# Kernel optimization log

Hardware: AMD Instinct MI355X
Metric: run time of the kernel (lower is better)

Reference implementation:

```python
import jax, jax.numpy as jnp
import numpy as np

B, N, C = 2, 4096, 512
NUM_HEADS = 8
HEAD_DIM = C // NUM_HEADS
SCALE = HEAD_DIM ** -0.5
THETA = 10000.0


def setup_inputs() -> dict:
    key = jax.random.key(0)
    ks = jax.random.split(key, 5)
    x = jax.random.normal(ks[0], (B, N, C), dtype=jnp.float32)
    Wqkv = jax.random.normal(ks[1], (3 * C, C), dtype=jnp.float32) * 0.02
    bqkv = jax.random.normal(ks[2], (3 * C,), dtype=jnp.float32) * 0.02
    Wproj = jax.random.normal(ks[3], (C, C), dtype=jnp.float32) * 0.02
    bproj = jax.random.normal(ks[4], (C,), dtype=jnp.float32) * 0.02
    return {"x": x, "Wqkv": Wqkv, "bqkv": bqkv, "Wproj": Wproj, "bproj": bproj}


def _rope(x, seq_len, head_dim):
    # x: [B, H, N, head_dim]; interleaved rotary embedding
    freqs = 1.0 / THETA ** (jnp.arange(0, head_dim, 2, dtype=jnp.float32) / head_dim)  # [hd/2]
    t = jnp.arange(seq_len, dtype=jnp.float32)
    freqs_cis = jnp.outer(t, freqs)                      # [N, hd/2]
    sin_f = jnp.sin(freqs_cis)
    cos_f = jnp.cos(freqs_cis)
    x_even = x[..., ::2]                                 # [B, H, N, hd/2]
    x_odd = x[..., 1::2]
    rot = jnp.stack(
        [x_even * cos_f - x_odd * sin_f,
         x_even * sin_f + x_odd * cos_f],
        axis=-1,
    )                                                    # [B, H, N, hd/2, 2]
    return rot.reshape(x.shape)


def reference(x, Wqkv, bqkv, Wproj, bproj):
    b, n, c = x.shape
    # fused QKV projection: y = x @ W.T + b
    qkv = x @ Wqkv.T + bqkv                              # [B, N, 3C]
    qkv = qkv.reshape(b, n, 3, NUM_HEADS, HEAD_DIM)
    qkv = jnp.transpose(qkv, (2, 0, 3, 1, 4))            # [3, B, H, N, hd]
    q, k, v = qkv[0], qkv[1], qkv[2]
    q = _rope(q, n, HEAD_DIM)
    k = _rope(k, n, HEAD_DIM)
    attn = jnp.einsum('bhqd,bhkd->bhqk', q, k) * SCALE   # [B, H, N, N]
    attn = jax.nn.softmax(attn, axis=-1)
    out = jnp.einsum('bhqk,bhkd->bhqd', attn, v)         # [B, H, N, hd]
    out = jnp.transpose(out, (0, 2, 1, 3)).reshape(b, n, c)
    return out @ Wproj.T + bproj
```

## Files before the change

### kernel.cpp

```cpp
#include <hip/hip_runtime.h>
#include <hip/hip_bf16.h>
#include <stdint.h>

#define B_ 2
#define N_ 4096
#define C_ 512
#define H_ 8
#define D_ 64
#define M_ (B_*N_)
#define K3_ (3*C_)
#define NCH 2

typedef __attribute__((ext_vector_type(8)))  short short8;
typedef __attribute__((ext_vector_type(4)))  float f32x4;
typedef __attribute__((ext_vector_type(16))) float f32x16;

static __device__ __forceinline__ unsigned short f2bf(float f) {
  union { float f; unsigned u; } cv; cv.f = f;
  unsigned r = cv.u + 0x7fffu + ((cv.u >> 16) & 1u);
  return (unsigned short)(r >> 16);
}
static __device__ __forceinline__ float bf2f(short x) {
  union { unsigned u; float f; } cv;
  cv.u = ((unsigned)(unsigned short)x) << 16;
  return cv.f;
}
static __device__ __forceinline__ float fexp2(float x) {
#if __has_builtin(__builtin_amdgcn_exp2f)
  return __builtin_amdgcn_exp2f(x);
#else
  return exp2f(x);
#endif
}
static __device__ __forceinline__ unsigned cvt_pk_bf16(float a, float b) {
  unsigned r;
  asm("v_cvt_pk_bf16_f32 %0, %1, %2" : "=v"(r) : "v"(a), "v"(b));
  return r;
}
static __device__ __forceinline__ void gload_lds16(const void* g, void* l) {
  __builtin_amdgcn_global_load_lds((const __attribute__((address_space(1))) unsigned*)g,
                                   (__attribute__((address_space(3))) unsigned*)l, 16, 0, 0);
}
static __device__ __forceinline__ f32x16 zero16() {
  f32x16 z;
#pragma unroll
  for (int i = 0; i < 16; i++) z[i] = 0.f;
  return z;
}

__global__ void prep(const float* __restrict__ x, const float* __restrict__ Wqkv,
                     const float* __restrict__ Wproj,
                     short* __restrict__ xb, short* __restrict__ wqkvb,
                     short* __restrict__ wprjb, float2* __restrict__ tab) {
  int blk = blockIdx.x, t = threadIdx.x;
  if (blk < 4096) {
    int i = blk * 256 + t;
    float4 v = ((const float4*)x)[i];
    short4 o;
    o.x = (short)f2bf(v.x); o.y = (short)f2bf(v.y);
    o.z = (short)f2bf(v.z); o.w = (short)f2bf(v.w);
    ((short4*)xb)[i] = o;
  } else if (blk < 4864) {
    int i = (blk - 4096) * 256 + t;
    float4 v = ((const float4*)Wqkv)[i];
    short4 o;
    o.x = (short)f2bf(v.x); o.y = (short)f2bf(v.y);
    o.z = (short)f2bf(v.z); o.w = (short)f2bf(v.w);
    ((short4*)wqkvb)[i] = o;
  } else if (blk < 5120) {
    int i = (blk - 4864) * 256 + t;
    float4 v = ((const float4*)Wproj)[i];
    short4 o;
    o.x = (short)f2bf(v.x); o.y = (short)f2bf(v.y);
    o.z = (short)f2bf(v.z); o.w = (short)f2bf(v.w);
    ((short4*)wprjb)[i] = o;
  } else {
    int i = (blk - 5120) * 256 + t;
    int p = i & 31, n = i >> 5;
    float freq = exp2f(-((float)(2 * p) / 64.0f) * 13.287712379549449f);
    float ang = (float)n * freq;
    float s, c;
    sincosf(ang, &s, &c);
    float2 r; r.x = c; r.y = s;
    tab[i] = r;
  }
}

__global__ void rope_vt(const short* __restrict__ qkvb, const float2* __restrict__ tab,
                        short* __restrict__ Qf, short* __restrict__ Kf,
                        short* __restrict__ Vf) {
  __shared__ short tile[128][72];
  int blk = blockIdx.x, t = threadIdx.x;
  if (blk < 1024) {
    int tk = blk >> 9;
    int bh = (blk & 511) >> 5;
    int nb4 = blk & 31;
    int b = bh >> 3, h = bh & 7;
    int n0 = nb4 * 128;
#pragma unroll
    for (int pass = 0; pass < 4; pass++) {
      int row = pass * 32 + (t >> 3), chunk = t & 7;
      short8 v = *(const short8*)(qkvb + (size_t)(b * N_ + n0 + row) * K3_ + tk * C_ + h * D_ + chunk * 8);
      *(short8*)&tile[row][chunk * 8] = v;
    }
    __syncthreads();
    int lane = t & 63, f = t >> 6;
    int c = lane & 31, hi = lane >> 5;
    int d0 = f * 16 + hi * 8;
    float sc = (tk == 0) ? 0.18033688011112042f : 1.0f;
    short* base = (tk ? Kf : Qf);
#pragma unroll
    for (int i = 0; i < 4; i++) {
      int n_l = i * 32 + c;
      short8 v = *(const short8*)&tile[n_l][d0];
      const float2* tp = tab + (size_t)(n0 + n_l) * 32 + (d0 >> 1);
      short8 w;
#pragma unroll
      for (int j = 0; j < 4; j++) {
        float e = bf2f(v[2 * j]), o = bf2f(v[2 * j + 1]);
        float2 cs = tp[j];
        float e2 = (e * cs.x - o * cs.y) * sc;
        float o2 = (e * cs.y + o * cs.x) * sc;
        w[2 * j] = (short)f2bf(e2);
        w[2 * j + 1] = (short)f2bf(o2);
      }
      short* dst = base + (((size_t)(bh * 128 + nb4 * 4 + i) * 4 + f) * 512) + lane * 8;
      *(short8*)dst = w;
    }
  } else {
    int blk2 = blk - 1024;
    int bh = blk2 >> 7, kblk = blk2 & 127;
    int b = bh >> 3, h = bh & 7;
    int n0 = kblk * 32;
    {
      int row = t >> 3, c8 = t & 7;
      short8 v = *(const short8*)(qkvb + (size_t)(b * N_ + n0 + row) * K3_ + 2 * C_ + h * D_ + c8 * 8);
      *(short8*)&tile[row][c8 * 8] = v;
    }
    __syncthreads();
    {
      int frag = t >> 6, lane = t & 63;
      int hi = lane >> 5, c = lane & 31;
      int g = frag & 1, dblk = frag >> 1;
      short8 w;
#pragma unroll
      for (int j = 0; j < 8; j++) w[j] = tile[g * 16 + hi * 8 + j][dblk * 32 + c];
      *(short8*)(Vf + ((size_t)(bh * 128 + kblk) * 4 + frag) * 512 + lane * 8) = w;
    }
  }
}

__global__ __launch_bounds__(256) void gemm_qkv(const short* __restrict__ A, const short* __restrict__ Bw,
                                                const float* __restrict__ bias, short* __restrict__ Cout,
                                                int M, int Nout, int K) {
  __shared__ short As[4 * 32 * 64];
  __shared__ short Bs[128 * 64];
  int t = threadIdx.x, lane = t & 63, w = t >> 6, wr = w >> 1, wc = w & 1;
  int tM = blockIdx.x * 128, tN = blockIdx.y * 128;
  int lrow = lane & 15, lhi = lane >> 4;
  int rs = (lrow & 7) * 8;
  f32x4 acc[4][4];
#pragma unroll
  for (int fm = 0; fm < 4; fm++)
#pragma unroll
    for (int fn = 0; fn < 4; fn++)
#pragma unroll
      for (int r = 0; r < 4; r++) acc[fm][fn][r] = 0.f;

  int srow = t >> 3;
  int sq = ((t & 7) * 8) ^ ((srow & 7) * 8);

  for (int k0 = 0; k0 < K; k0 += 64) {
#pragma unroll
    for (int p = 0; p < 4; p++)
      gload_lds16(A + (size_t)(tM + p * 32 + srow) * K + k0 + sq, As + p * 2048 + t * 8);
#pragma unroll
    for (int p = 0; p < 4; p++)
      gload_lds16(Bw + (size_t)(tN + p * 32 + srow) * K + k0 + sq, Bs + p * 2048 + t * 8);
    __syncthreads();
#pragma unroll
    for (int kk = 0; kk < 2; kk++) {
      int ko = (kk * 32 + lhi * 8) ^ rs;
      short8 af[4], bfr[4];
#pragma unroll
      for (int f = 0; f < 4; f++)
        af[f] = *(const short8*)(As + (wr * 64 + f * 16 + lrow) * 64 + ko);
#pragma unroll
      for (int f = 0; f < 4; f++)
        bfr[f] = *(const short8*)(Bs + (wc * 64 + f * 16 + lrow) * 64 + ko);
#pragma unroll
      for (int fm = 0; fm < 4; fm++)
#pragma unroll
        for (int fn = 0; fn < 4; fn++)
          acc[fm][fn] = __builtin_amdgcn_mfma_f32_16x16x32_bf16(af[fm], bfr[fn], acc[fm][fn], 0, 0, 0);
    }
    __syncthreads();
  }

#pragma unroll
  for (int fn = 0; fn < 4; fn++) {
    int col = tN + wc * 64 + fn * 16 + lrow;
    float bv = bias[col];
#pragma unroll
    for (int fm = 0; fm < 4; fm++) {
      int row0 = tM + wr * 64 + fm * 16 + lhi * 4;
#pragma unroll
      for (int r = 0; r < 4; r++) {
        float v = acc[fm][fn][r] + bv;
        Cout[(size_t)(row0 + r) * Nout + col] = (short)f2bf(v);
      }
    }
  }
}

__global__ __launch_bounds__(256) void gemm_proj(const short* __restrict__ Op, const float* __restrict__ lp,
                                                 const short* __restrict__ Bw, const float* __restrict__ bias,
                                                 float* __restrict__ Cout) {
  __shared__ short As[2 * 32 * 64];
  __shared__ short Bs[128 * 64];
  const size_t chs = (size_t)16 * N_ * D_;
  int t = threadIdx.x, lane = t & 63, w = t >> 6, wr = w >> 1, wc = w & 1;
  int tM = blockIdx.x * 64, tN = blockIdx.y * 128;
  int lrow = lane & 15, lhi = lane >> 4;
  int rs = (lrow & 7) * 8;
  f32x4 acc[2][4];
#pragma unroll
  for (int fm = 0; fm < 2; fm++)
#pragma unroll
    for (int fn = 0; fn < 4; fn++)
#pragma unroll
      for (int r = 0; r < 4; r++) acc[fm][fn][r] = 0.f;

  int srow = t >> 3;
  int sq = ((t & 7) * 8) ^ ((srow & 7) * 8);

  for (int k0 = 0; k0 < C_; k0 += 64) {
    int h = k0 >> 6;
#pragma unroll
    for (int p = 0; p < 2; p++) {
      int m = tM + p * 32 + srow;
      int b = m >> 12, q = m & (N_ - 1);
      size_t lidx = (size_t)(b * H_ + h) * N_ + q;
      float l = lp[lidx] + lp[(size_t)16 * N_ + lidx];
      float inv = 1.0f / l;
      size_t obase = ((size_t)(b * H_ + h) * N_ + q) * D_ + sq;
      short8 v0 = *(const short8*)(Op + obase);
      short8 v1 = *(const short8*)(Op + chs + obase);
      short8 wv;
#pragma unroll
      for (int j = 0; j < 8; j++) wv[j] = (short)f2bf((bf2f(v0[j]) + bf2f(v1[j])) * inv);
      *(short8*)(As + p * 2048 + t * 8) = wv;
    }
#pragma unroll
    for (int p = 0; p < 4; p++)
      gload_lds16(Bw + (size_t)(tN + p * 32 + srow) * C_ + k0 + sq, Bs + p * 2048 + t * 8);
    __syncthreads();
#pragma unroll
    for (int kk = 0; kk < 2; kk++) {
      int ko = (kk * 32 + lhi * 8) ^ rs;
      short8 af[2], bfr[4];
#pragma unroll
      for (int f = 0; f < 2; f++)
        af[f] = *(const short8*)(As + (wr * 32 + f * 16 + lrow) * 64 + ko);
#pragma unroll
      for (int f = 0; f < 4; f++)
        bfr[f] = *(const short8*)(Bs + (wc * 64 + f * 16 + lrow) * 64 + ko);
#pragma unroll
      for (int fm = 0; fm < 2; fm++)
#pragma unroll
        for (int fn = 0; fn < 4; fn++)
          acc[fm][fn] = __builtin_amdgcn_mfma_f32_16x16x32_bf16(af[fm], bfr[fn], acc[fm][fn], 0, 0, 0);
    }
    __syncthreads();
  }

#pragma unroll
  for (int fn = 0; fn < 4; fn++) {
    int col = tN + wc * 64 + fn * 16 + lrow;
    float bv = bias[col];
#pragma unroll
    for (int fm = 0; fm < 2; fm++) {
      int row0 = tM + wr * 32 + fm * 16 + lhi * 4;
#pragma unroll
      for (int r = 0; r < 4; r++)
        Cout[(size_t)(row0 + r) * C_ + col] = acc[fm][fn][r] + bv;
    }
  }
}

static __device__ __forceinline__ f32x16 qk4(const short8* k, const short8* q, const f32x16& z0) {
  __builtin_amdgcn_s_setprio(1);
  f32x16 st = __builtin_amdgcn_mfma_f32_32x32x16_bf16(k[0], q[0], z0, 0, 0, 0);
  st = __builtin_amdgcn_mfma_f32_32x32x16_bf16(k[1], q[1], st, 0, 0, 0);
  st = __builtin_amdgcn_mfma_f32_32x32x16_bf16(k[2], q[2], st, 0, 0, 0);
  st = __builtin_amdgcn_mfma_f32_32x32x16_bf16(k[3], q[3], st, 0, 0, 0);
  __builtin_amdgcn_s_setprio(0);
  return st;
}
static __device__ __forceinline__ void soft_pv(const f32x16& st, const short8* v,
                                               f32x16& o0, f32x16& o1, float& lsum) {
  float ls = 0.f;
  unsigned cpk[8];
#pragma unroll
  for (int q2 = 0; q2 < 4; q2++) {
    float e0 = fexp2(st[4 * q2]),     e1 = fexp2(st[4 * q2 + 1]);
    float e2 = fexp2(st[4 * q2 + 2]), e3 = fexp2(st[4 * q2 + 3]);
    ls += (e0 + e1) + (e2 + e3);
    cpk[2 * q2]     = cvt_pk_bf16(e0, e1);
    cpk[2 * q2 + 1] = cvt_pk_bf16(e2, e3);
  }
  lsum += ls;
  unsigned w00 = cpk[0], w02 = cpk[2];
  asm volatile("v_permlane32_swap_b32 %0, %1" : "+v"(w00), "+v"(w02));
  unsigned w01 = cpk[1], w03 = cpk[3];
  asm volatile("v_permlane32_swap_b32 %0, %1" : "+v"(w01), "+v"(w03));
  unsigned w10 = cpk[4], w12 = cpk[6];
  asm volatile("v_permlane32_swap_b32 %0, %1" : "+v"(w10), "+v"(w12));
  unsigned w11 = cpk[5], w13 = cpk[7];
  asm volatile("v_permlane32_swap_b32 %0, %1" : "+v"(w11), "+v"(w13));
  union { unsigned u[4]; short8 s; } u0, u1;
  u0.u[0] = w00; u0.u[1] = w01; u0.u[2] = w02; u0.u[3] = w03;
  u1.u[0] = w10; u1.u[1] = w11; u1.u[2] = w12; u1.u[3] = w13;
  __builtin_amdgcn_s_setprio(1);
  o0 = __builtin_amdgcn_mfma_f32_32x32x16_bf16(u0.s, v[0], o0, 0, 0, 0);
  o0 = __builtin_amdgcn_mfma_f32_32x32x16_bf16(u1.s, v[1], o0, 0, 0, 0);
  o1 = __builtin_amdgcn_mfma_f32_32x32x16_bf16(u0.s, v[2], o1, 0, 0, 0);
  o1 = __builtin_amdgcn_mfma_f32_32x32x16_bf16(u1.s, v[3], o1, 0, 0, 0);
  __builtin_amdgcn_s_setprio(0);
}

__global__ __launch_bounds__(256, 2) void attn(const short* __restrict__ Qf, const short* __restrict__ Kf,
                                               const short* __restrict__ Vf,
                                               short* __restrict__ Op, float* __restrict__ lp) {
  __shared__ short Ks[2][4096];
  __shared__ short Vs[2][4096];
  int bh = blockIdx.x;
  int ch = blockIdx.z;
  int t = threadIdx.x;
  int wv = t >> 6, lane = t & 63;
  int c = lane & 31, hi = lane >> 5;
  int q0 = blockIdx.y * 256 + wv * 64;
  const int nkb2 = N_ / (NCH * 64);
  int kb0 = ch * (N_ / (NCH * 32));

  const short* QbA = Qf + ((size_t)(bh * 128 + (q0 >> 5)) * 4) * 512 + lane * 8;
  const short* Kg = Kf + ((size_t)(bh * 128 + kb0) * 4) * 512 + t * 8;
  const short* Vg = Vf + ((size_t)(bh * 128 + kb0) * 4) * 512 + t * 8;

  short8 qA[4], qB[4];
#pragma unroll
  for (int f = 0; f < 4; f++) qA[f] = *(const short8*)(QbA + f * 512);
#pragma unroll
  for (int f = 0; f < 4; f++) qB[f] = *(const short8*)(QbA + (4 + f) * 512);

  const f32x16 z0 = zero16();
  f32x16 oA0 = z0, oA1 = z0;
  f32x16 oB0 = z0, oB1 = z0;
  float lsA = 0.f, lsB = 0.f;

  gload_lds16(Kg,        &Ks[0][t * 8]);
  gload_lds16(Kg + 2048, &Ks[0][2048 + t * 8]);
  gload_lds16(Vg,        &Vs[0][t * 8]);
  gload_lds16(Vg + 2048, &Vs[0][2048 + t * 8]);
  __syncthreads();

  int buf = 0;
  for (int it = 0; it < nkb2; ++it) {
    if (it + 1 < nkb2) {
      const short* Kn = Kg + (size_t)(it + 1) * 4096;
      const short* Vn = Vg + (size_t)(it + 1) * 4096;
      gload_lds16(Kn,        &Ks[buf ^ 1][t * 8]);
      gload_lds16(Kn + 2048, &Ks[buf ^ 1][2048 + t * 8]);
      gload_lds16(Vn,        &Vs[buf ^ 1][t * 8]);
      gload_lds16(Vn + 2048, &Vs[buf ^ 1][2048 + t * 8]);
    }
#pragma unroll
    for (int s = 0; s < 2; s++) {
      short8 kf[4], vf[4];
#pragma unroll
      for (int f = 0; f < 4; f++) kf[f] = *(const short8*)&Ks[buf][s * 2048 + f * 512 + lane * 8];
#pragma unroll
      for (int f = 0; f < 4; f++) vf[f] = *(const short8*)&Vs[buf][s * 2048 + f * 512 + lane * 8];
      f32x16 stA = qk4(kf, qA, z0);
      f32x16 stB = qk4(kf, qB, z0);
      soft_pv(stA, vf, oA0, oA1, lsA);
      soft_pv(stB, vf, oB0, oB1, lsB);
    }
    __syncthreads();
    buf ^= 1;
  }

  float ltA = lsA + __shfl_xor(lsA, 32);
  float ltB = lsB + __shfl_xor(lsB, 32);
  float* lrow = lp + ((size_t)ch * 16 + bh) * N_ + q0;
  short* obase = Op + ((size_t)ch * 16 + bh) * N_ * D_;
  if (hi == 0) {
    lrow[c] = ltA;
    lrow[32 + c] = ltB;
  }
#pragma unroll
  for (int r = 0; r < 16; r++) {
    int ql = (r & 3) + 8 * (r >> 2) + 4 * hi;
    size_t nA = (size_t)(q0 + ql) * D_;
    size_t nB = (size_t)(q0 + 32 + ql) * D_;
    obase[nA + c]      = (short)f2bf(oA0[r]);
    obase[nA + 32 + c] = (short)f2bf(oA1[r]);
    obase[nB + c]      = (short)f2bf(oB0[r]);
    obase[nB + 32 + c] = (short)f2bf(oB1[r]);
  }
}

extern "C" void kernel_launch(void* const* d_in, const int* in_sizes, int n_in,
                              void* d_out, int out_size, void* d_ws, size_t ws_size,
                              hipStream_t stream) {
  const float* x     = (const float*)d_in[0];
  const float* Wqkv  = (const float*)d_in[1];
  const float* bqkv  = (const float*)d_in[2];
  const float* Wproj = (const float*)d_in[3];
  const float* bproj = (const float*)d_in[4];
  float* out = (float*)d_out;
  char* ws = (char*)d_ws;

  const size_t off_wprjb = 0;
  const size_t off_tab   = 524288;
  const size_t off_q     = 1572864;
  const size_t off_k     = 9961472;
  const size_t off_vt    = 18350080;
  const size_t off_xb    = 35127296;
  const size_t off_wqkvb = 43515904;
  const size_t off_qkvb  = 45088768;
  const size_t off_op    = 35127296;
  const size_t off_l     = 68681728;
  if (ws_size < 70254592) return;

  short* xb    = (short*)(ws + off_xb);
  short* wqkvb = (short*)(ws + off_wqkvb);
  short* wprjb = (short*)(ws + off_wprjb);
  short* qkvb  = (short*)(ws + off_qkvb);
  short* Qfp   = (short*)(ws + off_q);
  short* Kfp   = (short*)(ws + off_k);
  short* Vfp   = (short*)(ws + off_vt);
  float2* tab  = (float2*)(ws + off_tab);
  short* Opp   = (short*)(ws + off_op);
  float* lpp   = (float*)(ws + off_l);

  prep<<<dim3(5632), dim3(256), 0, stream>>>(x, Wqkv, Wproj, xb, wqkvb, wprjb, tab);

  gemm_qkv<<<dim3(64, 12), dim3(256), 0, stream>>>(xb, wqkvb, bqkv, qkvb, M_, K3_, C_);

  rope_vt<<<dim3(3072), dim3(256), 0, stream>>>(qkvb, tab, Qfp, Kfp, Vfp);

  attn<<<dim3(16, 16, NCH), dim3(256), 0, stream>>>(Qfp, Kfp, Vfp, Opp, lpp);

  gemm_proj<<<dim3(128, 4), dim3(256), 0, stream>>>(Opp, lpp, wprjb, bproj, out);
}
```

Baseline: 135.9 us.

## Fuse RoPE and V transpose into QKV GEMM epilogue, drop rope_vt kernel

The QKV GEMM epilogue now applies bias, rotary embedding (pairing even/odd columns via lane shuffle) and Q scaling. It writes Q, K and V straight into the fragment layouts the attention kernel expects, so the intermediate qkv buffer and the separate rope_vt launch go away. This removes one kernel launch and a full write-then-read of the bf16 QKV tensor. In exchange the epilogue does scattered 2-byte stores for Q/K and short4 stores for V, which may coalesce poorly.

```diff
diff --git a/kernel.cpp b/kernel.cpp
--- a/kernel.cpp
+++ b/kernel.cpp
@@ -86,75 +86,13 @@
   }
 }
 
-__global__ void rope_vt(const short* __restrict__ qkvb, const float2* __restrict__ tab,
-                        short* __restrict__ Qf, short* __restrict__ Kf,
-                        short* __restrict__ Vf) {
-  __shared__ short tile[128][72];
-  int blk = blockIdx.x, t = threadIdx.x;
-  if (blk < 1024) {
-    int tk = blk >> 9;
-    int bh = (blk & 511) >> 5;
-    int nb4 = blk & 31;
-    int b = bh >> 3, h = bh & 7;
-    int n0 = nb4 * 128;
-#pragma unroll
-    for (int pass = 0; pass < 4; pass++) {
-      int row = pass * 32 + (t >> 3), chunk = t & 7;
-      short8 v = *(const short8*)(qkvb + (size_t)(b * N_ + n0 + row) * K3_ + tk * C_ + h * D_ + chunk * 8);
-      *(short8*)&tile[row][chunk * 8] = v;
-    }
-    __syncthreads();
-    int lane = t & 63, f = t >> 6;
-    int c = lane & 31, hi = lane >> 5;
-    int d0 = f * 16 + hi * 8;
-    float sc = (tk == 0) ? 0.18033688011112042f : 1.0f;
-    short* base = (tk ? Kf : Qf);
-#pragma unroll
-    for (int i = 0; i < 4; i++) {
-      int n_l = i * 32 + c;
-      short8 v = *(const short8*)&tile[n_l][d0];
-      const float2* tp = tab + (size_t)(n0 + n_l) * 32 + (d0 >> 1);
-      short8 w;
-#pragma unroll
-      for (int j = 0; j < 4; j++) {
-        float e = bf2f(v[2 * j]), o = bf2f(v[2 * j + 1]);
-        float2 cs = tp[j];
-        float e2 = (e * cs.x - o * cs.y) * sc;
-        float o2 = (e * cs.y + o * cs.x) * sc;
-        w[2 * j] = (short)f2bf(e2);
-        w[2 * j + 1] = (short)f2bf(o2);
-      }
-      short* dst = base + (((size_t)(bh * 128 + nb4 * 4 + i) * 4 + f) * 512) + lane * 8;
-      *(short8*)dst = w;
-    }
-  } else {
-    int blk2 = blk - 1024;
-    int bh = blk2 >> 7, kblk = blk2 & 127;
-    int b = bh >> 3, h = bh & 7;
-    int n0 = kblk * 32;
-    {
-      int row = t >> 3, c8 = t & 7;
-      short8 v = *(const short8*)(qkvb + (size_t)(b * N_ + n0 + row) * K3_ + 2 * C_ + h * D_ + c8 * 8);
-      *(short8*)&tile[row][c8 * 8] = v;
-    }
-    __syncthreads();
-    {
-      int frag = t >> 6, lane = t & 63;
-      int hi = lane >> 5, c = lane & 31;
-      int g = frag & 1, dblk = frag >> 1;
-      short8 w;
-#pragma unroll
-      for (int j = 0; j < 8; j++) w[j] = tile[g * 16 + hi * 8 + j][dblk * 32 + c];
-      *(short8*)(Vf + ((size_t)(bh * 128 + kblk) * 4 + frag) * 512 + lane * 8) = w;
-    }
-  }
-}
-
 __global__ __launch_bounds__(256) void gemm_qkv(const short* __restrict__ A, const short* __restrict__ Bw,
-                                                const float* __restrict__ bias, short* __restrict__ Cout,
-                                                int M, int Nout, int K) {
+                                                const float* __restrict__ bias, const float2* __restrict__ tab,
+                                                short* __restrict__ Qf, short* __restrict__ Kf,
+                                                short* __restrict__ Vf) {
   __shared__ short As[4 * 32 * 64];
   __shared__ short Bs[128 * 64];
+  const int K = C_;
   int t = threadIdx.x, lane = t & 63, w = t >> 6, wr = w >> 1, wc = w & 1;
   int tM = blockIdx.x * 128, tN = blockIdx.y * 128;
   int lrow = lane & 15, lhi = lane >> 4;
@@ -197,17 +135,53 @@
     __syncthreads();
   }
 
-#pragma unroll
-  for (int fn = 0; fn < 4; fn++) {
-    int col = tN + wc * 64 + fn * 16 + lrow;
-    float bv = bias[col];
-#pragma unroll
-    for (int fm = 0; fm < 4; fm++) {
-      int row0 = tM + wr * 64 + fm * 16 + lhi * 4;
-#pragma unroll
-      for (int r = 0; r < 4; r++) {
-        float v = acc[fm][fn][r] + bv;
-        Cout[(size_t)(row0 + r) * Nout + col] = (short)f2bf(v);
+  if (blockIdx.y < 8) {
+#pragma unroll
+    for (int fn = 0; fn < 4; fn++) {
+      int col = tN + wc * 64 + fn * 16 + lrow;
+      float bv = bias[col];
+      int tk = col >> 9;
+      int h = (col >> 6) & 7;
+      int d = col & 63;
+      float sc = tk ? 1.0f : 0.18033688011112042f;
+      short* basep = tk ? Kf : Qf;
+      bool even = ((d & 1) == 0);
+#pragma unroll
+      for (int fm = 0; fm < 4; fm++) {
+#pragma unroll
+        for (int r = 0; r < 4; r++) {
+          int m = tM + wr * 64 + fm * 16 + lhi * 4 + r;
+          int b = m >> 12, n = m & (N_ - 1);
+          float v = acc[fm][fn][r] + bv;
+          float pv = __shfl_xor(v, 1);
+          float2 cs = tab[(size_t)n * 32 + (d >> 1)];
+          float e = even ? v : pv, o = even ? pv : v;
+          float outv = (even ? (e * cs.x - o * cs.y) : (e * cs.y + o * cs.x)) * sc;
+          size_t flat = ((size_t)(((b * H_ + h) * 128 + (n >> 5)) * 4 + (d >> 4))) * 512
+                        + ((d >> 3) & 1) * 256 + (n & 31) * 8 + (d & 7);
+          basep[flat] = (short)f2bf(outv);
+        }
+      }
+    }
+  } else {
+#pragma unroll
+    for (int fn = 0; fn < 4; fn++) {
+      int col = tN + wc * 64 + fn * 16 + lrow;
+      float bv = bias[col];
+      int h = (col >> 6) & 7;
+      int d = col & 63;
+#pragma unroll
+      for (int fm = 0; fm < 4; fm++) {
+        int m0 = tM + wr * 64 + fm * 16 + lhi * 4;
+        int b = m0 >> 12, n0 = m0 & (N_ - 1);
+        size_t flat0 = ((size_t)(((b * H_ + h) * 128 + (n0 >> 5)) * 4 + (d >> 5) * 2 + ((n0 >> 4) & 1))) * 512
+                       + ((n0 >> 3) & 1) * 256 + (d & 31) * 8 + (n0 & 7);
+        short4 w4;
+        w4.x = (short)f2bf(acc[fm][fn][0] + bv);
+        w4.y = (short)f2bf(acc[fm][fn][1] + bv);
+        w4.z = (short)f2bf(acc[fm][fn][2] + bv);
+        w4.w = (short)f2bf(acc[fm][fn][3] + bv);
+        *(short4*)(Vf + flat0) = w4;
       }
     }
   }
@@ -428,15 +402,13 @@
   const size_t off_vt    = 18350080;
   const size_t off_xb    = 35127296;
   const size_t off_wqkvb = 43515904;
-  const size_t off_qkvb  = 45088768;
-  const size_t off_op    = 35127296;
+  const size_t off_op    = 45088768;
   const size_t off_l     = 68681728;
   if (ws_size < 70254592) return;
 
   short* xb    = (short*)(ws + off_xb);
   short* wqkvb = (short*)(ws + off_wqkvb);
   short* wprjb = (short*)(ws + off_wprjb);
-  short* qkvb  = (short*)(ws + off_qkvb);
   short* Qfp   = (short*)(ws + off_q);
   short* Kfp   = (short*)(ws + off_k);
   short* Vfp   = (short*)(ws + off_vt);
@@ -446,9 +418,7 @@
 
   prep<<<dim3(5632), dim3(256), 0, stream>>>(x, Wqkv, Wproj, xb, wqkvb, wprjb, tab);
 
-  gemm_qkv<<<dim3(64, 12), dim3(256), 0, stream>>>(xb, wqkvb, bqkv, qkvb, M_, K3_, C_);
-
-  rope_vt<<<dim3(3072), dim3(256), 0, stream>>>(qkvb, tab, Qfp, Kfp, Vfp);
+  gemm_qkv<<<dim3(64, 12), dim3(256), 0, stream>>>(xb, wqkvb, bqkv, tab, Qfp, Kfp, Vfp);
 
   attn<<<dim3(16, 16, NCH), dim3(256), 0, stream>>>(Qfp, Kfp, Vfp, Opp, lpp);
 
```

New measurement: 125.7 us (median of 2 runs). 1.08x faster.
